# Performance work log

Hardware: AMD Instinct MI355X
Metric: run time of the kernel (lower is better)

Reference implementation:

```python
import jax, jax.numpy as jnp
import numpy as np

EMBED_DIM = 1024
NUM_HEADS = 16
HEAD_DIM = EMBED_DIM // NUM_HEADS
B, T = 4, 2048


def setup_inputs() -> dict:
    key = jax.random.key(0)
    ks = jax.random.split(key, 10)
    s = 1.0 / np.sqrt(EMBED_DIM)
    inp = {
        "x": jax.random.normal(ks[0], (B, T, EMBED_DIM), dtype=jnp.float32),
        "mask": jnp.ones((B, T), dtype=bool),
        "q_w": jax.random.uniform(ks[1], (EMBED_DIM, EMBED_DIM), jnp.float32, -s, s),
        "q_b": jax.random.uniform(ks[2], (EMBED_DIM,), jnp.float32, -s, s),
        "k_w": jax.random.uniform(ks[3], (EMBED_DIM, EMBED_DIM), jnp.float32, -s, s),
        "k_b": jax.random.uniform(ks[4], (EMBED_DIM,), jnp.float32, -s, s),
        "v_w": jax.random.uniform(ks[5], (EMBED_DIM, EMBED_DIM), jnp.float32, -s, s),
        "v_b": jax.random.uniform(ks[6], (EMBED_DIM,), jnp.float32, -s, s),
        "o_w": jax.random.uniform(ks[7], (EMBED_DIM, EMBED_DIM), jnp.float32, -s, s),
        "o_b": jax.random.uniform(ks[8], (EMBED_DIM,), jnp.float32, -s, s),
    }
    return inp


def reference(x, mask, q_w, q_b, k_w, k_b, v_w, v_b, o_w, o_b):
    # NOTE: original module accepts `mask` but never uses it; dropout defined but never applied.
    Bn, Tn, C = x.shape
    H, D = NUM_HEADS, HEAD_DIM
    # Linear: x @ W.T + b, then split heads -> [B, H, T, D]
    Q = (x @ q_w.T + q_b).reshape(Bn, Tn, H, D).transpose(0, 2, 1, 3)
    K = (x @ k_w.T + k_b).reshape(Bn, Tn, H, D).transpose(0, 2, 1, 3)
    V = (x @ v_w.T + v_b).reshape(Bn, Tn, H, D).transpose(0, 2, 1, 3)
    scores = jnp.einsum("bhqd,bhkd->bhqk", Q, K) / jnp.sqrt(jnp.float32(D))
    attn = jax.nn.softmax(scores, axis=-1)
    out = jnp.einsum("bhqk,bhkd->bhqd", attn, V)
    out = out.transpose(0, 2, 1, 3).reshape(Bn, Tn, C)
    return out @ o_w.T + o_b
```

## Files before the change

### kernel.cpp

```cpp
#include <hip/hip_runtime.h>
#include <stdint.h>

#define B_ 4
#define T_ 2048
#define C_ 1024
#define H_ 16
#define D_ 64
#define CK 1024

typedef __attribute__((ext_vector_type(8))) short bf8;
typedef __attribute__((ext_vector_type(4))) float f4;

__device__ __forceinline__ ushort f2bf(float f) {
  union { float f; uint32_t u; } c; c.f = f;
  uint32_t u = c.u;
  uint32_t r = (u + 0x7fffu + ((u >> 16) & 1u)) >> 16;
  return (ushort)r;
}

__device__ __forceinline__ uint32_t cvtpk(float a, float b) {
  uint32_t r;
  asm("v_cvt_pk_bf16_f32 %0, %1, %2" : "=v"(r) : "v"(a), "v"(b));
  return r;
}

__global__ __launch_bounds__(256) void cast_all(const float* __restrict__ x,
                                                const float* __restrict__ w0,
                                                const float* __restrict__ w1,
                                                const float* __restrict__ w2,
                                                const float* __restrict__ w3,
                                                ushort* __restrict__ xo,
                                                ushort* __restrict__ o0,
                                                ushort* __restrict__ o1,
                                                ushort* __restrict__ o2,
                                                ushort* __restrict__ o3) {
  int bid = blockIdx.x;
  const float* in;
  ushort* out;
  int lb;
  if (bid < 8192) {
    in = x; out = xo; lb = bid;
  } else {
    int wsel = (bid - 8192) >> 10;
    lb = (bid - 8192) & 1023;
    switch (wsel) {
      case 0: in = w0; out = o0; break;
      case 1: in = w1; out = o1; break;
      case 2: in = w2; out = o2; break;
      default: in = w3; out = o3; break;
    }
  }
  int i = (lb * 256 + threadIdx.x) * 4;
  float4 v = *(const float4*)(in + i);
  ushort4 o;
  o.x = f2bf(v.x); o.y = f2bf(v.y); o.z = f2bf(v.z); o.w = f2bf(v.w);
  *(ushort4*)(out + i) = o;
}

__global__ __launch_bounds__(512, 2) void gemm8(const ushort* __restrict__ A,
                                                const ushort* __restrict__ W,
                                                const float* __restrict__ b0,
                                                const float* __restrict__ b1,
                                                const float* __restrict__ b2,
                                                void* __restrict__ outp,
                                                int mode, float qsc) {
  extern __shared__ ushort smem[];
  ushort* sA = smem;
  ushort* sB = smem + 16384;

  const int tid = threadIdx.x;
  const int w = tid >> 6, l = tid & 63, lo = l & 15, hi = l >> 4;
  const int wm = w >> 2, wn = w & 3;

  const int i = blockIdx.x;
  const int m0 = ((i & 7) * 8 + ((i >> 3) & 7)) * 128;
  const int n0 = (i >> 6) * 256;

  const int rl = tid >> 3, c7 = tid & 7;
  const int scol = (c7 ^ (rl & 7)) * 8;
  const ushort* Asrc = A + (size_t)(m0 + rl) * CK + scol;
  const int Brow0 = ((rl >> 5) * 64) + (rl & 31);
  const ushort* Bsrc = W + (size_t)(n0 + Brow0) * CK + scol;
  const int Bdst0 = Brow0 * 64 + c7 * 8;

  const int sw0 = (hi ^ (lo & 7)) * 8;
  const int sw1 = ((4 + hi) ^ (lo & 7)) * 8;
  const int arow = wm * 64 + lo;
  const int brow = wn * 64 + lo;

  f4 acc[4][4];
#pragma unroll
  for (int f = 0; f < 4; ++f)
#pragma unroll
    for (int g = 0; g < 4; ++g) acc[f][g] = (f4){0.f, 0.f, 0.f, 0.f};

#define GL(src, dst) __builtin_amdgcn_global_load_lds(                                   \
      (const __attribute__((address_space(1))) void*)(src),                              \
      (__attribute__((address_space(3))) void*)(dst), 16, 0, 0)
#define STG_A(nb, kn) {                                                                  \
    GL(Asrc + (kn),                    &sA[(nb)*8192 + tid*8]);                          \
    GL(Asrc + (kn) + (size_t)64 * CK,  &sA[(nb)*8192 + 4096 + tid*8]); }
#define STG_B(nb, h, kn) {                                                               \
    GL(Bsrc + (kn) + (size_t)((h)*32) * CK,        &sB[(nb)*16384 + (h)*2048 + Bdst0]);           \
    GL(Bsrc + (kn) + (size_t)((h)*32 + 128) * CK,  &sB[(nb)*16384 + (h)*2048 + 8192 + Bdst0]); }
#define VMC(s)  asm volatile("s_waitcnt vmcnt(" s ")" ::: "memory")
#define PH_BAR  { __builtin_amdgcn_s_barrier(); asm volatile("" ::: "memory"); }
#define LDA_H(cb, hh) {                                                                  \
  _Pragma("unroll")                                                                      \
  for (int f = (hh)*2; f < (hh)*2 + 2; ++f) {                                            \
    af[f][0] = *(const bf8*)&sA[(cb)*8192 + (arow + f*16)*64 + sw0];                     \
    af[f][1] = *(const bf8*)&sA[(cb)*8192 + (arow + f*16)*64 + sw1]; } }
#define LDB(cb, dst, h) {                                                                \
  _Pragma("unroll")                                                                      \
  for (int g = 0; g < 2; ++g) {                                                          \
    dst[g][0] = *(const bf8*)&sB[(cb)*16384 + (brow + (h)*32 + g*16)*64 + sw0];          \
    dst[g][1] = *(const bf8*)&sB[(cb)*16384 + (brow + (h)*32 + g*16)*64 + sw1]; } }
#define MM8(fo, go, bfr) {                                                               \
  __builtin_amdgcn_s_setprio(1);                                                         \
  _Pragma("unroll")                                                                      \
  for (int f = (fo); f < (fo) + 2; ++f)                                                  \
    _Pragma("unroll")                                                                    \
    for (int g = 0; g < 2; ++g) {                                                        \
      acc[f][(go)+g] = __builtin_amdgcn_mfma_f32_16x16x32_bf16(af[f][0], bfr[g][0], acc[f][(go)+g], 0, 0, 0); \
      acc[f][(go)+g] = __builtin_amdgcn_mfma_f32_16x16x32_bf16(af[f][1], bfr[g][1], acc[f][(go)+g], 0, 0, 0); } \
  __builtin_amdgcn_s_setprio(0); }

  bf8 af[4][2], bA[2][2], bB[2][2];

  STG_A(0, 0); STG_B(0, 0, 0); STG_B(0, 1, 0);
  VMC("0"); PH_BAR;
  int cur = 0;

  for (int t = 0; t < (CK / 64) - 1; ++t) {
    const int nb = cur ^ 1;
    const int kn = (t + 1) * 64;
    LDA_H(cur, 0); LDB(cur, bA, 0);
    STG_A(nb, kn);
    VMC("4"); PH_BAR;
    MM8(0, 0, bA); PH_BAR;
    LDA_H(cur, 1);
    STG_B(nb, 0, kn);
    PH_BAR;
    MM8(2, 0, bA); PH_BAR;
    LDB(cur, bB, 1);
    STG_B(nb, 1, kn);
    VMC("6"); PH_BAR;
    MM8(0, 2, bB); PH_BAR;
    MM8(2, 2, bB); PH_BAR;
    cur = nb;
  }
  VMC("0"); PH_BAR;
  LDA_H(cur, 0); LDB(cur, bA, 0); MM8(0, 0, bA);
  LDA_H(cur, 1);                  MM8(2, 0, bA);
  LDB(cur, bB, 1);                MM8(0, 2, bB);
                                  MM8(2, 2, bB);
#undef GL
#undef STG_A
#undef STG_B
#undef VMC
#undef PH_BAR
#undef LDA_H
#undef LDB
#undef MM8

  if (mode == 0) {
    float* O = (float*)outp;
#pragma unroll
    for (int f = 0; f < 4; ++f)
#pragma unroll
      for (int gn = 0; gn < 4; ++gn) {
        int n = n0 + wn * 64 + gn * 16 + lo;
        float bv = b0[n];
#pragma unroll
        for (int j = 0; j < 4; ++j) {
          int m = m0 + wm * 64 + f * 16 + hi * 4 + j;
          O[(size_t)m * C_ + n] = acc[f][gn][j] + bv;
        }
      }
  } else {
    const int proj = n0 >> 10;
    if (proj < 2) {
      const float* bp = (proj == 0) ? b0 : b1;
      const float os = (proj == 0) ? qsc : 1.0f;
      ushort* O = (ushort*)outp + (size_t)proj * (8u << 20);
#pragma unroll
      for (int f = 0; f < 4; ++f)
#pragma unroll
        for (int gn = 0; gn < 4; ++gn) {
          int n = n0 + wn * 64 + gn * 16 + lo;
          int nl = n & 1023;
          int h = nl >> 6, d = nl & 63;
          float bv = bp[nl];
#pragma unroll
          for (int j = 0; j < 4; ++j) {
            int m = m0 + wm * 64 + f * 16 + hi * 4 + j;
            int b = m >> 11, t = m & 2047;
            O[(size_t)((b << 4) + h) * (T_ * D_) + t * D_ + d] = f2bf((acc[f][gn][j] + bv) * os);
          }
        }
    } else {
      ushort* O = (ushort*)outp + (size_t)2 * (8u << 20);
#pragma unroll
      for (int f = 0; f < 4; ++f)
#pragma unroll
        for (int gn = 0; gn < 4; ++gn) {
          int n = n0 + wn * 64 + gn * 16 + lo;
          int nl = n & 1023;
          int h = nl >> 6, d = nl & 63;
          float bv = b2[nl];
          int mb = m0 + wm * 64 + f * 16 + hi * 4;
          int b = mb >> 11, t = mb & 2047;
          ushort4 pk;
          pk.x = f2bf(acc[f][gn][0] + bv);
          pk.y = f2bf(acc[f][gn][1] + bv);
          pk.z = f2bf(acc[f][gn][2] + bv);
          pk.w = f2bf(acc[f][gn][3] + bv);
          *(ushort4*)&O[((size_t)((b << 4) + h) * D_ + d) * T_ + t] = pk;
        }
    }
  }
}

__global__ __launch_bounds__(256, 4) void attn_kernel(const ushort* __restrict__ Q,
                                                      const ushort* __restrict__ Kg,
                                                      const ushort* __restrict__ VT,
                                                      ushort* __restrict__ O) {
  __shared__ ushort Ks[2][64 * 64];
  __shared__ ushort Vs[2][64 * 64];

  const int tid = threadIdx.x;
  const int w = tid >> 6, l = tid & 63, lo = l & 15, hi = l >> 4;
  const int linear = blockIdx.y * 16 + blockIdx.x;
  const int bh = (linear & 7) * 8 + ((linear >> 3) & 7);
  const int q0 = (linear >> 6) * 128 + w * 32;
  const ushort* Qb  = Q  + (size_t)bh * T_ * D_;
  const ushort* Kb  = Kg + (size_t)bh * T_ * D_;
  const ushort* VTb = VT + (size_t)bh * D_ * T_;

  bf8 qf[2][2];
#pragma unroll
  for (int qs = 0; qs < 2; ++qs)
#pragma unroll
    for (int c = 0; c < 2; ++c)
      qf[qs][c] = *(const bf8*)&Qb[(q0 + qs * 16 + lo) * D_ + c * 32 + hi * 8];

  f4 o[2][4], accL[2];
#pragma unroll
  for (int qs = 0; qs < 2; ++qs) {
    accL[qs] = (f4){0.f, 0.f, 0.f, 0.f};
#pragma unroll
    for (int dt = 0; dt < 4; ++dt) o[qs][dt] = (f4){0.f, 0.f, 0.f, 0.f};
  }
  const short ONE = 0x3F80;
  const bf8 ones = (bf8){ONE, ONE, ONE, ONE, ONE, ONE, ONE, ONE};

  const int rowA  = tid >> 3;
  const int colsw = ((tid & 7) ^ (rowA & 7)) * 8;
  const int permA = ((rowA >> 2) & 3) * 8 + ((rowA >> 4) & 1) * 4 + (rowA & 3);
  const ushort* Ksrc0 = Kb  + (size_t)permA * D_ + colsw;
  const ushort* Ksrc1 = Kb  + (size_t)(32 + permA) * D_ + colsw;
  const ushort* Vsrc0 = VTb + (size_t)rowA * T_ + colsw;
  const ushort* Vsrc1 = VTb + (size_t)(rowA + 32) * T_ + colsw;

  const int swz = (lo & 7) << 3;
  const int NT = T_ / 64;

#define STAGE(b, kvo)                                                                              \
  {                                                                                                \
    __builtin_amdgcn_global_load_lds((const __attribute__((address_space(1))) void*)(Ksrc0 + (size_t)(kvo) * D_), \
                                     (__attribute__((address_space(3))) void*)&Ks[b][tid * 8], 16, 0, 0);          \
    __builtin_amdgcn_global_load_lds((const __attribute__((address_space(1))) void*)(Ksrc1 + (size_t)(kvo) * D_), \
                                     (__attribute__((address_space(3))) void*)&Ks[b][2048 + tid * 8], 16, 0, 0);   \
    __builtin_amdgcn_global_load_lds((const __attribute__((address_space(1))) void*)(Vsrc0 + (kvo)),               \
                                     (__attribute__((address_space(3))) void*)&Vs[b][tid * 8], 16, 0, 0);          \
    __builtin_amdgcn_global_load_lds((const __attribute__((address_space(1))) void*)(Vsrc1 + (kvo)),               \
                                     (__attribute__((address_space(3))) void*)&Vs[b][2048 + tid * 8], 16, 0, 0);   \
  }

  STAGE(0, 0);
  __syncthreads();
  int cur = 0;

  for (int t = 0; t < NT; ++t) {
    if (t + 1 < NT) STAGE(cur ^ 1, (t + 1) * 64);

    const ushort* Kc = &Ks[cur][0];
    const ushort* Vc = &Vs[cur][0];

    bf8 kf[4][2], vf[4][2];
#pragma unroll
    for (int n = 0; n < 4; ++n) {
      kf[n][0] = *(const bf8*)&Kc[(n * 16 + lo) * 64 + ((hi * 8) ^ swz)];
      kf[n][1] = *(const bf8*)&Kc[(n * 16 + lo) * 64 + ((32 + hi * 8) ^ swz)];
    }
#pragma unroll
    for (int dt = 0; dt < 4; ++dt) {
      vf[dt][0] = *(const bf8*)&Vc[(dt * 16 + lo) * 64 + ((hi * 8) ^ swz)];
      vf[dt][1] = *(const bf8*)&Vc[(dt * 16 + lo) * 64 + ((32 + hi * 8) ^ swz)];
    }

#pragma unroll
    for (int qs = 0; qs < 2; ++qs) {
      f4 z[4];
#pragma unroll
      for (int n = 0; n < 4; ++n) {
        f4 zz = (f4){0.f, 0.f, 0.f, 0.f};
        zz = __builtin_amdgcn_mfma_f32_16x16x32_bf16(kf[n][0], qf[qs][0], zz, 0, 0, 0);
        zz = __builtin_amdgcn_mfma_f32_16x16x32_bf16(kf[n][1], qf[qs][1], zz, 0, 0, 0);
        z[n] = zz;
      }

      uint32_t pd[8];
#pragma unroll
      for (int n = 0; n < 4; ++n) {
        float e0 = __builtin_amdgcn_exp2f(z[n][0]);
        float e1 = __builtin_amdgcn_exp2f(z[n][1]);
        float e2 = __builtin_amdgcn_exp2f(z[n][2]);
        float e3 = __builtin_amdgcn_exp2f(z[n][3]);
        pd[n * 2 + 0] = cvtpk(e0, e1);
        pd[n * 2 + 1] = cvtpk(e2, e3);
      }
      union U8 { uint32_t u[4]; bf8 v; } u0, u1;
      u0.u[0] = pd[0]; u0.u[1] = pd[1]; u0.u[2] = pd[2]; u0.u[3] = pd[3];
      u1.u[0] = pd[4]; u1.u[1] = pd[5]; u1.u[2] = pd[6]; u1.u[3] = pd[7];

      accL[qs] = __builtin_amdgcn_mfma_f32_16x16x32_bf16(u0.v, ones, accL[qs], 0, 0, 0);
      accL[qs] = __builtin_amdgcn_mfma_f32_16x16x32_bf16(u1.v, ones, accL[qs], 0, 0, 0);

#pragma unroll
      for (int dt = 0; dt < 4; ++dt) {
        o[qs][dt] = __builtin_amdgcn_mfma_f32_16x16x32_bf16(u0.v, vf[dt][0], o[qs][dt], 0, 0, 0);
        o[qs][dt] = __builtin_amdgcn_mfma_f32_16x16x32_bf16(u1.v, vf[dt][1], o[qs][dt], 0, 0, 0);
      }
    }

    __syncthreads();
    cur ^= 1;
  }
#undef STAGE

  const int b = bh >> 4, h = bh & 15;
#pragma unroll
  for (int qs = 0; qs < 2; ++qs)
#pragma unroll
    for (int j = 0; j < 4; ++j) {
      float invL = 1.0f / accL[qs][j];
      int q = q0 + qs * 16 + hi * 4 + j;
#pragma unroll
      for (int dt = 0; dt < 4; ++dt)
        O[(size_t)(b * T_ + q) * C_ + h * D_ + dt * 16 + lo] = f2bf(o[qs][dt][j] * invL);
    }
}

extern "C" void kernel_launch(void* const* d_in, const int* in_sizes, int n_in,
                              void* d_out, int out_size, void* d_ws, size_t ws_size,
                              hipStream_t stream) {
  const float* x  = (const float*)d_in[0];
  const float* qw = (const float*)d_in[2];
  const float* qb = (const float*)d_in[3];
  const float* kw = (const float*)d_in[4];
  const float* kb = (const float*)d_in[5];
  const float* vw = (const float*)d_in[6];
  const float* vb = (const float*)d_in[7];
  const float* ow = (const float*)d_in[8];
  const float* ob = (const float*)d_in[9];
  float* out = (float*)d_out;

  char* ws = (char*)d_ws;
  ushort* xbf   = (ushort*)ws;
  ushort* qwbf  = (ushort*)(ws + (16u << 20));
  ushort* kwbf  = qwbf + (1u << 20);
  ushort* vwbf  = kwbf + (1u << 20);
  ushort* owbf  = vwbf + (1u << 20);
  ushort* Qws   = (ushort*)(ws + (24u << 20));
  ushort* VTws  = (ushort*)(ws + (56u << 20));
  ushort* attnw = (ushort*)(ws + (72u << 20));

  hipFuncSetAttribute((const void*)gemm8, hipFuncAttributeMaxDynamicSharedMemorySize, 98304);

  cast_all<<<12288, 256, 0, stream>>>(x, qw, kw, vw, ow, xbf, qwbf, kwbf, vwbf, owbf);

  const float QSC = 0.125f * 1.44269504f;
  gemm8<<<768, 512, 98304, stream>>>(xbf, qwbf, qb, kb, vb, Qws, 1, QSC);

  attn_kernel<<<dim3(T_ / 128, B_ * H_), 256, 0, stream>>>(Qws, Qws + (size_t)(8u << 20), VTws, attnw);

  gemm8<<<256, 512, 98304, stream>>>(attnw, owbf, ob, nullptr, nullptr, out, 0, 1.0f);
}
```

Measured before the change: 162.7 us.

## Add 128x384-tile QKV projection GEMM kernel with split-phase B staging

Adds a dedicated QKV projection GEMM that uses 128x384 output tiles, giving 512 blocks instead of the previous 768-block gemm8 launch. B-tile loading and MFMA work are split into two phases so that half of the next stage loads while the current half computes. Epilogue writes Q/K head-major and V transposed with bias and scaling. The kernel uses 128KB of shared memory per block and more accumulators, which can lower occupancy and raise register pressure. 512 blocks also leave a partial second wave on the GPU.

```diff
diff --git a/kernel.cpp b/kernel.cpp
--- a/kernel.cpp
+++ b/kernel.cpp
@@ -55,6 +55,138 @@
   ushort4 o;
   o.x = f2bf(v.x); o.y = f2bf(v.y); o.z = f2bf(v.z); o.w = f2bf(v.w);
   *(ushort4*)(out + i) = o;
+}
+
+__global__ __launch_bounds__(512, 2) void gemm384(const ushort* __restrict__ A,
+                                                  const ushort* __restrict__ W,
+                                                  const float* __restrict__ b0,
+                                                  const float* __restrict__ b1,
+                                                  const float* __restrict__ b2,
+                                                  ushort* __restrict__ outp,
+                                                  float qsc) {
+  extern __shared__ ushort smem[];
+  ushort* sA = smem;
+  ushort* sB = smem + 16384;
+
+  const int tid = threadIdx.x;
+  const int w = tid >> 6, l = tid & 63, lo = l & 15, hi = l >> 4;
+  const int wm = w >> 2, wn = w & 3;
+
+  const int i = blockIdx.x;
+  const int m0 = ((i & 7) * 8 + ((i >> 3) & 7)) * 128;
+  const int n0 = (i >> 6) * 384;
+
+  const int rl = tid >> 3, c7 = tid & 7;
+  const int scol = (c7 ^ (rl & 7)) * 8;
+  const ushort* Asrc = A + (size_t)(m0 + rl) * CK + scol;
+  const ushort* Bsrc = W + (size_t)(n0 + rl) * CK + scol;
+
+  const int sw0 = (hi ^ (lo & 7)) * 8;
+  const int sw1 = ((4 + hi) ^ (lo & 7)) * 8;
+  const int arow = wm * 64 + lo;
+  const int brow = wn * 96 + lo;
+
+  f4 acc[4][6];
+#pragma unroll
+  for (int f = 0; f < 4; ++f)
+#pragma unroll
+    for (int g = 0; g < 6; ++g) acc[f][g] = (f4){0.f, 0.f, 0.f, 0.f};
+
+#define GL(src, dst) __builtin_amdgcn_global_load_lds(                                   \
+      (const __attribute__((address_space(1))) void*)(src),                              \
+      (__attribute__((address_space(3))) void*)(dst), 16, 0, 0)
+#define STG_A(nb, kn) {                                                                  \
+    GL(Asrc + (kn),                    &sA[(nb)*8192 + tid*8]);                          \
+    GL(Asrc + (kn) + (size_t)64 * CK,  &sA[(nb)*8192 + 4096 + tid*8]); }
+#define STG_B3(nb, h, kn) {                                                              \
+    GL(Bsrc + (kn) + (size_t)(((h)*3 + 0) * 64) * CK, &sB[(nb)*24576 + ((h)*3 + 0)*4096 + tid*8]); \
+    GL(Bsrc + (kn) + (size_t)(((h)*3 + 1) * 64) * CK, &sB[(nb)*24576 + ((h)*3 + 1)*4096 + tid*8]); \
+    GL(Bsrc + (kn) + (size_t)(((h)*3 + 2) * 64) * CK, &sB[(nb)*24576 + ((h)*3 + 2)*4096 + tid*8]); }
+#define VMC(s)  asm volatile("s_waitcnt vmcnt(" s ")" ::: "memory")
+#define PH_BAR  { __builtin_amdgcn_s_barrier(); asm volatile("" ::: "memory"); }
+#define LDA(cb) {                                                                        \
+  _Pragma("unroll")                                                                      \
+  for (int f = 0; f < 4; ++f) {                                                          \
+    af[f][0] = *(const bf8*)&sA[(cb)*8192 + (arow + f*16)*64 + sw0];                     \
+    af[f][1] = *(const bf8*)&sA[(cb)*8192 + (arow + f*16)*64 + sw1]; } }
+#define LDB3(cb, dst, h) {                                                               \
+  _Pragma("unroll")                                                                      \
+  for (int g = 0; g < 3; ++g) {                                                          \
+    dst[g][0] = *(const bf8*)&sB[(cb)*24576 + (brow + ((h)*3 + g)*16)*64 + sw0];         \
+    dst[g][1] = *(const bf8*)&sB[(cb)*24576 + (brow + ((h)*3 + g)*16)*64 + sw1]; } }
+#define MM24(h, bfr) {                                                                   \
+  __builtin_amdgcn_s_setprio(1);                                                         \
+  _Pragma("unroll")                                                                      \
+  for (int f = 0; f < 4; ++f)                                                            \
+    _Pragma("unroll")                                                                    \
+    for (int g = 0; g < 3; ++g) {                                                        \
+      acc[f][(h)*3+g] = __builtin_amdgcn_mfma_f32_16x16x32_bf16(af[f][0], bfr[g][0], acc[f][(h)*3+g], 0, 0, 0); \
+      acc[f][(h)*3+g] = __builtin_amdgcn_mfma_f32_16x16x32_bf16(af[f][1], bfr[g][1], acc[f][(h)*3+g], 0, 0, 0); } \
+  __builtin_amdgcn_s_setprio(0); }
+
+  bf8 af[4][2], bA[3][2], bB[3][2];
+
+  STG_A(0, 0); STG_B3(0, 0, 0); STG_B3(0, 1, 0);
+  VMC("0"); PH_BAR;
+  int cur = 0;
+
+  for (int t = 0; t < (CK / 64) - 1; ++t) {
+    const int nb = cur ^ 1;
+    const int kn = (t + 1) * 64;
+    LDA(cur); LDB3(cur, bA, 0);
+    STG_A(nb, kn); STG_B3(nb, 0, kn);
+    VMC("8"); PH_BAR;
+    MM24(0, bA); PH_BAR;
+    LDB3(cur, bB, 1);
+    STG_B3(nb, 1, kn);
+    VMC("8"); PH_BAR;
+    MM24(1, bB); PH_BAR;
+    cur = nb;
+  }
+  VMC("0"); PH_BAR;
+  LDA(cur); LDB3(cur, bA, 0); MM24(0, bA);
+  LDB3(cur, bB, 1);           MM24(1, bB);
+#undef GL
+#undef STG_A
+#undef STG_B3
+#undef VMC
+#undef PH_BAR
+#undef LDA
+#undef LDB3
+#undef MM24
+
+#pragma unroll
+  for (int f = 0; f < 4; ++f)
+#pragma unroll
+    for (int gn = 0; gn < 6; ++gn) {
+      int n = n0 + wn * 96 + gn * 16 + lo;
+      int proj = n >> 10;
+      int nl = n & 1023;
+      int h = nl >> 6, d = nl & 63;
+      if (proj < 2) {
+        const float* bp = (proj == 0) ? b0 : b1;
+        const float os = (proj == 0) ? qsc : 1.0f;
+        ushort* O = outp + (size_t)proj * (8u << 20);
+        float bv = bp[nl];
+#pragma unroll
+        for (int j = 0; j < 4; ++j) {
+          int m = m0 + wm * 64 + f * 16 + hi * 4 + j;
+          int b = m >> 11, t = m & 2047;
+          O[(size_t)((b << 4) + h) * (T_ * D_) + t * D_ + d] = f2bf((acc[f][gn][j] + bv) * os);
+        }
+      } else {
+        ushort* O = outp + (size_t)2 * (8u << 20);
+        float bv = b2[nl];
+        int mb = m0 + wm * 64 + f * 16 + hi * 4;
+        int b = mb >> 11, t = mb & 2047;
+        ushort4 pk;
+        pk.x = f2bf(acc[f][gn][0] + bv);
+        pk.y = f2bf(acc[f][gn][1] + bv);
+        pk.z = f2bf(acc[f][gn][2] + bv);
+        pk.w = f2bf(acc[f][gn][3] + bv);
+        *(ushort4*)&O[((size_t)((b << 4) + h) * D_ + d) * T_ + t] = pk;
+      }
+    }
 }
 
 __global__ __launch_bounds__(512, 2) void gemm8(const ushort* __restrict__ A,
@@ -376,12 +508,13 @@
   ushort* VTws  = (ushort*)(ws + (56u << 20));
   ushort* attnw = (ushort*)(ws + (72u << 20));
 
+  hipFuncSetAttribute((const void*)gemm384, hipFuncAttributeMaxDynamicSharedMemorySize, 131072);
   hipFuncSetAttribute((const void*)gemm8, hipFuncAttributeMaxDynamicSharedMemorySize, 98304);
 
   cast_all<<<12288, 256, 0, stream>>>(x, qw, kw, vw, ow, xbf, qwbf, kwbf, vwbf, owbf);
 
   const float QSC = 0.125f * 1.44269504f;
-  gemm8<<<768, 512, 98304, stream>>>(xbf, qwbf, qb, kb, vb, Qws, 1, QSC);
+  gemm384<<<512, 512, 131072, stream>>>(xbf, qwbf, qb, kb, vb, Qws, QSC);
 
   attn_kernel<<<dim3(T_ / 128, B_ * H_), 256, 0, stream>>>(Qws, Qws + (size_t)(8u << 20), VTws, attnw);
 
```

Measured after the change: 167.7 us. 3.1% more time.
